# Kernel optimization log

Hardware: AMD Instinct MI355X
Metric: run time of the kernel (lower is better)

The kernel has to match this reference:

```python
import jax, jax.numpy as jnp
import numpy as np

D_MODEL = 1024
NUM_HEADS = 16
D_K = D_MODEL // NUM_HEADS
LOCAL_WINDOW = 16
LOCALITY_STRENGTH = 2.0


def _xavier(key, shape):
    fan_in, fan_out = shape[1], shape[0]
    a = jnp.sqrt(6.0 / (fan_in + fan_out))
    return jax.random.uniform(key, shape, jnp.float32, -a, a)


def setup_inputs() -> dict:
    key = jax.random.key(0)
    ks = jax.random.split(key, 9)
    B, S = 4, 2048
    query = jax.random.normal(ks[0], (B, S, D_MODEL), jnp.float32)
    key_t = jax.random.normal(ks[1], (B, S, D_MODEL), jnp.float32)
    value = jax.random.normal(ks[2], (B, S, D_MODEL), jnp.float32)
    wq = _xavier(ks[3], (D_MODEL, D_MODEL))
    wk = _xavier(ks[4], (D_MODEL, D_MODEL))
    wv = _xavier(ks[5], (D_MODEL, D_MODEL))
    wo = _xavier(ks[6], (D_MODEL, D_MODEL))
    bq = jnp.zeros((D_MODEL,), jnp.float32)
    bk = jnp.zeros((D_MODEL,), jnp.float32)
    bv = jnp.zeros((D_MODEL,), jnp.float32)
    bo = jnp.zeros((D_MODEL,), jnp.float32)
    # learned local relative-position bias, length 2*W+1; randomize so grads/math are nontrivial
    local_bias = 0.02 * jax.random.normal(ks[7], (2 * LOCAL_WINDOW + 1,), jnp.float32)
    return {"query": query, "key": key_t, "value": value,
            "wq": wq, "bq": bq, "wk": wk, "bk": bk, "wv": wv, "bv": bv,
            "wo": wo, "bo": bo, "local_bias": local_bias}


def _local_bias_matrix(local_bias, seq_len):
    # bias[i, j] = local_bias[j - i + W] if |j - i| <= W else 0  (banded)
    i = jnp.arange(seq_len)
    rel = i[None, :] - i[:, None]                 # [S, S]
    valid = jnp.abs(rel) <= LOCAL_WINDOW
    idx = jnp.clip(rel + LOCAL_WINDOW, 0, 2 * LOCAL_WINDOW)
    return jnp.where(valid, local_bias[idx], 0.0)  # [S, S]


def reference(query, key, value, wq, bq, wk, bk, wv, bv, wo, bo, local_bias):
    B, S, _ = query.shape
    H, Dk = NUM_HEADS, D_K
    q = (query @ wq.T + bq).reshape(B, S, H, Dk).transpose(0, 2, 1, 3)  # [B,H,S,Dk]
    k = (key @ wk.T + bk).reshape(B, S, H, Dk).transpose(0, 2, 1, 3)
    v = (value @ wv.T + bv).reshape(B, S, H, Dk).transpose(0, 2, 1, 3)
    scores = jnp.einsum('bhqd,bhkd->bhqk', q, k) / jnp.sqrt(jnp.float32(Dk))
    bias = _local_bias_matrix(local_bias, S)       # [S,S], broadcasts over [B,H]
    scores = scores + LOCALITY_STRENGTH * bias
    attn = jax.nn.softmax(scores, axis=-1)
    out = jnp.einsum('bhqk,bhkd->bhqd', attn, v)   # [B,H,S,Dk]
    out = out.transpose(0, 2, 1, 3).reshape(B, S, H * Dk)
    return out @ wo.T + bo
```

## Files before the change

### kernel.cpp

```cpp
#include <hip/hip_runtime.h>
#include <hip/hip_bf16.h>
#include <stdint.h>

typedef __bf16 bf16_t;
typedef bf16_t bf16x8 __attribute__((ext_vector_type(8)));
typedef bf16_t bf16x4 __attribute__((ext_vector_type(4)));
typedef float f32x4 __attribute__((ext_vector_type(4)));

#define LOG2E 1.44269504088896340736f

__device__ __forceinline__ void gld16(const void* g, void* l) {
  __builtin_amdgcn_global_load_lds(
      (__attribute__((address_space(1))) void*)(void*)(g),
      (__attribute__((address_space(3))) void*)(l), 16, 0, 0);
}

__device__ __forceinline__ int swz(int byteoff) {
  return byteoff ^ (((byteoff >> 7) & 7) << 4);
}

__global__ __launch_bounds__(256) void cvt7_kernel(
    const float* __restrict__ a0, const float* __restrict__ a1, const float* __restrict__ a2,
    const float* __restrict__ w0, const float* __restrict__ w1,
    const float* __restrict__ w2, const float* __restrict__ w3,
    bf16_t* __restrict__ e0, bf16_t* __restrict__ e1, bf16_t* __restrict__ e2,
    bf16_t* __restrict__ f0, bf16_t* __restrict__ f1,
    bf16_t* __restrict__ f2, bf16_t* __restrict__ f3) {
  const float* s;
  bf16_t* d;
  int i, stride;
  if (blockIdx.x < 3072) {
    const int t = blockIdx.x >> 10;
    s = (t == 0) ? a0 : ((t == 1) ? a1 : a2);
    d = (t == 0) ? e0 : ((t == 1) ? e1 : e2);
    i = (blockIdx.x & 1023) * 256 + threadIdx.x;
    stride = 1024 * 256;
  } else {
    const int b = blockIdx.x - 3072;
    const int t = b >> 7;
    s = (t == 0) ? w0 : ((t == 1) ? w1 : ((t == 2) ? w2 : w3));
    d = (t == 0) ? f0 : ((t == 1) ? f1 : ((t == 2) ? f2 : f3));
    i = (b & 127) * 256 + threadIdx.x;
    stride = 128 * 256;
  }
#pragma unroll
  for (int u = 0; u < 8; ++u, i += stride) {
    const float4 v = reinterpret_cast<const float4*>(s)[i];
    bf16x4 o;
    o[0] = (bf16_t)v.x; o[1] = (bf16_t)v.y; o[2] = (bf16_t)v.z; o[3] = (bf16_t)v.w;
    reinterpret_cast<bf16x4*>(d)[i] = o;
  }
}

#define GBM 128
#define GBN 128
#define GBK 64

__global__ __launch_bounds__(256) void gemm_qkv(
    const bf16_t* __restrict__ Xq, const bf16_t* __restrict__ Xk, const bf16_t* __restrict__ Xv,
    const bf16_t* __restrict__ Wq, const bf16_t* __restrict__ Wk, const bf16_t* __restrict__ Wv,
    const float* __restrict__ bq, const float* __restrict__ bk, const float* __restrict__ bv,
    bf16_t* __restrict__ Qo, bf16_t* __restrict__ Ko, bf16_t* __restrict__ Vo,
    int M, int N, int K) {
  const int z = blockIdx.z;
  const bf16_t* A = (z == 0) ? Xq : ((z == 1) ? Xk : Xv);
  const bf16_t* W = (z == 0) ? Wq : ((z == 1) ? Wk : Wv);
  const float* bias = (z == 0) ? bq : ((z == 1) ? bk : bv);
  bf16_t* Out = (z == 0) ? Qo : ((z == 1) ? Ko : Vo);

  __shared__ bf16_t As[GBM * GBK];
  __shared__ bf16_t Bs[GBN * GBK];
  const int tid = threadIdx.x;
  const int lane = tid & 63;
  const int w = tid >> 6;
  const int m0 = blockIdx.x * GBM;
  const int n0 = blockIdx.y * GBN;
  const int wm = (w >> 1) * 64;
  const int wn = (w & 1) * 64;

  f32x4 acc[4][4] = {};

  const int t16 = tid * 16;
  int srow[4], scb[4];
#pragma unroll
  for (int i = 0; i < 4; ++i) {
    const int so = swz(i * 4096 + t16);
    srow[i] = so >> 7;
    scb[i] = so & 127;
  }
  const char* Ab = (const char*)A;
  const char* Wb = (const char*)W;

  const int rr = lane & 15;
  const int kk8 = (lane >> 4) * 8;

  for (int k0 = 0; k0 < K; k0 += GBK) {
#pragma unroll
    for (int i = 0; i < 4; ++i) {
      gld16(Ab + ((size_t)(m0 + srow[i]) * K + k0) * 2 + scb[i], (char*)As + i * 4096 + t16);
      gld16(Wb + ((size_t)(n0 + srow[i]) * K + k0) * 2 + scb[i], (char*)Bs + i * 4096 + t16);
    }
    __syncthreads();
#pragma unroll
    for (int kk = 0; kk < 2; ++kk) {
      bf16x8 a[4], b[4];
#pragma unroll
      for (int i = 0; i < 4; ++i)
        a[i] = *reinterpret_cast<const bf16x8*>(
            (const char*)As + swz((wm + i * 16 + rr) * 128 + (kk * 32 + kk8) * 2));
#pragma unroll
      for (int i = 0; i < 4; ++i)
        b[i] = *reinterpret_cast<const bf16x8*>(
            (const char*)Bs + swz((wn + i * 16 + rr) * 128 + (kk * 32 + kk8) * 2));
#pragma unroll
      for (int i = 0; i < 4; ++i)
#pragma unroll
        for (int j = 0; j < 4; ++j)
          acc[i][j] = __builtin_amdgcn_mfma_f32_16x16x32_bf16(a[i], b[j], acc[i][j], 0, 0, 0);
    }
    __syncthreads();
  }

  const int rg = (lane >> 4) * 4;
#pragma unroll
  for (int i = 0; i < 4; ++i) {
#pragma unroll
    for (int j = 0; j < 4; ++j) {
      const int col = n0 + wn + j * 16 + rr;
      const float bi = bias[col];
      if (z == 2) {
        const int row0 = m0 + wm + i * 16 + rg;
        const int b_ = row0 >> 11, s_ = row0 & 2047;
        const int h_ = col >> 6, d_ = col & 63;
        const int k64 = s_ & 63;
        const int sl = (k64 & 32) | ((k64 & 12) << 1) | ((k64 & 16) >> 2);
        const int scol = (s_ & ~63) | sl;
        bf16x4 pack;
#pragma unroll
        for (int r = 0; r < 4; ++r) pack[r] = (bf16_t)(acc[i][j][r] + bi);
        *reinterpret_cast<bf16x4*>(&Out[((size_t)((b_ * 16 + h_) * 64 + d_)) * 2048 + scol]) = pack;
      } else {
        const float scale = (z == 0) ? (0.125f * LOG2E) : 1.0f;
#pragma unroll
        for (int r = 0; r < 4; ++r) {
          const int row = m0 + wm + i * 16 + rg + r;
          const int b_ = row >> 11, s_ = row & 2047;
          const int h_ = col >> 6, d_ = col & 63;
          Out[((size_t)((b_ * 16 + h_) * 2048 + s_)) * 64 + d_] = (bf16_t)((acc[i][j][r] + bi) * scale);
        }
      }
    }
  }
}

__global__ __launch_bounds__(256) void gemm_o(
    const bf16_t* __restrict__ A, const bf16_t* __restrict__ W,
    const float* __restrict__ bias, float* __restrict__ Out,
    int M, int N, int K) {
  __shared__ bf16_t As[GBM * GBK];
  __shared__ bf16_t Bs[GBN * GBK];
  const int tid = threadIdx.x;
  const int lane = tid & 63;
  const int w = tid >> 6;
  const int m0 = blockIdx.x * GBM;
  const int n0 = blockIdx.y * GBN;
  const int wm = (w >> 1) * 64;
  const int wn = (w & 1) * 64;

  f32x4 acc[4][4] = {};

  const int t16 = tid * 16;
  int srow[4], scb[4];
#pragma unroll
  for (int i = 0; i < 4; ++i) {
    const int so = swz(i * 4096 + t16);
    srow[i] = so >> 7;
    scb[i] = so & 127;
  }
  const char* Ab = (const char*)A;
  const char* Wb = (const char*)W;

  const int rr = lane & 15;
  const int kk8 = (lane >> 4) * 8;

  for (int k0 = 0; k0 < K; k0 += GBK) {
#pragma unroll
    for (int i = 0; i < 4; ++i) {
      gld16(Ab + ((size_t)(m0 + srow[i]) * K + k0) * 2 + scb[i], (char*)As + i * 4096 + t16);
      gld16(Wb + ((size_t)(n0 + srow[i]) * K + k0) * 2 + scb[i], (char*)Bs + i * 4096 + t16);
    }
    __syncthreads();
#pragma unroll
    for (int kk = 0; kk < 2; ++kk) {
      bf16x8 a[4], b[4];
#pragma unroll
      for (int i = 0; i < 4; ++i)
        a[i] = *reinterpret_cast<const bf16x8*>(
            (const char*)As + swz((wm + i * 16 + rr) * 128 + (kk * 32 + kk8) * 2));
#pragma unroll
      for (int i = 0; i < 4; ++i)
        b[i] = *reinterpret_cast<const bf16x8*>(
            (const char*)Bs + swz((wn + i * 16 + rr) * 128 + (kk * 32 + kk8) * 2));
#pragma unroll
      for (int i = 0; i < 4; ++i)
#pragma unroll
        for (int j = 0; j < 4; ++j)
          acc[i][j] = __builtin_amdgcn_mfma_f32_16x16x32_bf16(a[i], b[j], acc[i][j], 0, 0, 0);
    }
    __syncthreads();
  }

  const int rg = (lane >> 4) * 4;
#pragma unroll
  for (int i = 0; i < 4; ++i)
#pragma unroll
    for (int j = 0; j < 4; ++j) {
      const int col = n0 + wn + j * 16 + rr;
      const float bi = bias[col];
#pragma unroll
      for (int r = 0; r < 4; ++r) {
        const int row = m0 + wm + i * 16 + rg + r;
        Out[(size_t)row * N + col] = acc[i][j][r] + bi;
      }
    }
}

#define QT 256
#define KT 64

__global__ __launch_bounds__(256, 2) void attn_kernel(
    const bf16_t* __restrict__ Qg, const bf16_t* __restrict__ Kg,
    const bf16_t* __restrict__ Vtg, const float* __restrict__ lb,
    bf16_t* __restrict__ Og) {
  const int S = 2048;
  __shared__ bf16_t Qs[QT * 64];
  __shared__ bf16_t Ks[KT * 64];
  __shared__ bf16_t Vts[64 * KT];
  __shared__ float lbs[33];

  const int tid = threadIdx.x, lane = tid & 63, w = tid >> 6;
  const int bh = blockIdx.x;
  const int qt0 = blockIdx.y * QT;
  const int b_ = bh >> 4, h_ = bh & 15;

  const char* Qb = (const char*)(Qg + (size_t)bh * S * 64);
  const char* Kb = (const char*)(Kg + (size_t)bh * S * 64);
  const char* Vtb = (const char*)(Vtg + (size_t)bh * 64 * S);

#pragma unroll
  for (int i = 0; i < 8; ++i) {
    const int off = i * 4096 + tid * 16;
    gld16(Qb + (size_t)qt0 * 128 + swz(off), (char*)Qs + off);
  }
  if (tid < 33) lbs[tid] = lb[tid];

  const int L0 = tid * 16;
  const int W0 = swz(L0), W1 = swz(L0 + 4096);
  const int vd0 = L0 >> 7, vcb = L0 & 127;
  int4 kr0, kr1, vr0, vr1;

#define LOADKV(t)                                                              \
  {                                                                            \
    const char* kp = Kb + (size_t)(t) * 8192;                                  \
    kr0 = *reinterpret_cast<const int4*>(kp + L0);                             \
    kr1 = *reinterpret_cast<const int4*>(kp + L0 + 4096);                      \
    const char* vp = Vtb + (size_t)(t) * 128;                                  \
    vr0 = *reinterpret_cast<const int4*>(vp + (size_t)vd0 * 4096 + vcb);       \
    vr1 = *reinterpret_cast<const int4*>(vp + (size_t)(vd0 + 32) * 4096 + vcb);\
  }
#define WRITEKV()                                                              \
  {                                                                            \
    *reinterpret_cast<int4*>((char*)Ks + W0) = kr0;                            \
    *reinterpret_cast<int4*>((char*)Ks + W1) = kr1;                            \
    *reinterpret_cast<int4*>((char*)Vts + W0) = vr0;                           \
    *reinterpret_cast<int4*>((char*)Vts + W1) = vr1;                           \
  }

  LOADKV(0)
  __syncthreads();

  const int rr = lane & 15;
  const int kk8 = (lane >> 4) * 8;
  const int rg = (lane >> 4) * 4;

  bf16x8 qf[4][2];
#pragma unroll
  for (int qg = 0; qg < 4; ++qg)
#pragma unroll
    for (int kk = 0; kk < 2; ++kk) {
      const int off = (w * 64 + qg * 16 + rr) * 128 + (kk * 32 + kk8) * 2;
      qf[qg][kk] = *reinterpret_cast<const bf16x8*>((const char*)Qs + swz(off));
    }

  f32x4 oacc[4][4] = {};
  float lrowp[4] = {0.f, 0.f, 0.f, 0.f};

  for (int kt = 0; kt < S / KT; ++kt) {
    WRITEKV()
    __syncthreads();
    LOADKV((kt + 1) & 31)

    bf16x8 kf[4][2];
#pragma unroll
    for (int ni = 0; ni < 4; ++ni)
#pragma unroll
      for (int kk = 0; kk < 2; ++kk) {
        const int off = (ni * 16 + rr) * 128 + (kk * 32 + kk8) * 2;
        kf[ni][kk] = *reinterpret_cast<const bf16x8*>((const char*)Ks + swz(off));
      }
    bf16x8 vf[2][4];
#pragma unroll
    for (int kk = 0; kk < 2; ++kk)
#pragma unroll
      for (int nd = 0; nd < 4; ++nd) {
        const int off = (nd * 16 + rr) * 128 + (kk * 32 + kk8) * 2;
        vf[kk][nd] = *reinterpret_cast<const bf16x8*>((const char*)Vts + swz(off));
      }

    const int kbase = kt * KT;
#pragma unroll
    for (int qg = 0; qg < 4; ++qg) {
      f32x4 sc[4];
      __builtin_amdgcn_s_setprio(1);
#pragma unroll
      for (int ni = 0; ni < 4; ++ni) {
        f32x4 z = {0.f, 0.f, 0.f, 0.f};
#pragma unroll
        for (int kk = 0; kk < 2; ++kk)
          z = __builtin_amdgcn_mfma_f32_16x16x32_bf16(kf[ni][kk], qf[qg][kk], z, 0, 0, 0);
        sc[ni] = z;
      }
      __builtin_amdgcn_s_setprio(0);

      const int qlo = qt0 + w * 64 + qg * 16;
      if (kbase + KT + 16 > qlo && kbase < qlo + 16 + 16) {
        const int q = qlo + rr;
#pragma unroll
        for (int ni = 0; ni < 4; ++ni)
#pragma unroll
          for (int r = 0; r < 4; ++r) {
            const int rel = (kbase + ni * 16 + rg + r) - q;
            if (rel >= -16 && rel <= 16)
              sc[ni][r] += (2.0f * LOG2E) * lbs[rel + 16];
          }
      }

      bf16x8 paf[2];
      float ps0 = 0.f, ps1 = 0.f;
#pragma unroll
      for (int ni = 0; ni < 4; ++ni) {
        const float p0 = exp2f(sc[ni][0]);
        const float p1 = exp2f(sc[ni][1]);
        const float p2 = exp2f(sc[ni][2]);
        const float p3 = exp2f(sc[ni][3]);
        ps0 += p0 + p2;
        ps1 += p1 + p3;
        paf[ni >> 1][(ni & 1) * 4 + 0] = (bf16_t)p0;
        paf[ni >> 1][(ni & 1) * 4 + 1] = (bf16_t)p1;
        paf[ni >> 1][(ni & 1) * 4 + 2] = (bf16_t)p2;
        paf[ni >> 1][(ni & 1) * 4 + 3] = (bf16_t)p3;
      }
      lrowp[qg] += ps0 + ps1;

      __builtin_amdgcn_s_setprio(1);
#pragma unroll
      for (int kk = 0; kk < 2; ++kk)
#pragma unroll
        for (int nd = 0; nd < 4; ++nd)
          oacc[qg][nd] = __builtin_amdgcn_mfma_f32_16x16x32_bf16(paf[kk], vf[kk][nd], oacc[qg][nd], 0, 0, 0);
      __builtin_amdgcn_s_setprio(0);
    }
    __syncthreads();
  }

#pragma unroll
  for (int qg = 0; qg < 4; ++qg) {
    float t = lrowp[qg];
    t += __shfl_xor(t, 16, 64);
    t += __shfl_xor(t, 32, 64);
    float lf[4];
#pragma unroll
    for (int r = 0; r < 4; ++r)
      lf[r] = __shfl(t, (lane & 48) | (rg + r), 64);
#pragma unroll
    for (int nd = 0; nd < 4; ++nd)
#pragma unroll
      for (int r = 0; r < 4; ++r) {
        const int srow = qt0 + w * 64 + qg * 16 + rg + r;
        const int d = nd * 16 + rr;
        const float v = oacc[qg][nd][r] / lf[r];
        Og[((size_t)(b_ * 2048 + srow)) * 1024 + h_ * 64 + d] = (bf16_t)v;
      }
  }
}

extern "C" void kernel_launch(void* const* d_in, const int* in_sizes, int n_in,
                              void* d_out, int out_size, void* d_ws, size_t ws_size,
                              hipStream_t stream) {
  const float* q32 = (const float*)d_in[0];
  const float* k32 = (const float*)d_in[1];
  const float* v32 = (const float*)d_in[2];
  const float* wq = (const float*)d_in[3];
  const float* bq = (const float*)d_in[4];
  const float* wk = (const float*)d_in[5];
  const float* bk = (const float*)d_in[6];
  const float* wv = (const float*)d_in[7];
  const float* bv = (const float*)d_in[8];
  const float* wo = (const float*)d_in[9];
  const float* bo = (const float*)d_in[10];
  const float* lb = (const float*)d_in[11];

  const int M = 8192, N = 1024, K = 1024;
  const size_t REG = (size_t)M * N * 2;

  char* ws = (char*)d_ws;
  bf16_t* Xq = (bf16_t*)(ws + 0 * REG);
  bf16_t* Xk = (bf16_t*)(ws + 1 * REG);
  bf16_t* Xv = (bf16_t*)(ws + 2 * REG);
  bf16_t* Qb = (bf16_t*)(ws + 3 * REG);
  bf16_t* Wqb = (bf16_t*)(ws + 4 * REG);
  bf16_t* Wkb = Wqb + (size_t)N * K;
  bf16_t* Wvb = Wkb + (size_t)N * K;
  bf16_t* Wob = Wvb + (size_t)N * K;
  bf16_t* Kb = Xq;
  bf16_t* Vt = Xk;
  bf16_t* attn = Xv;

  cvt7_kernel<<<dim3(3584), dim3(256), 0, stream>>>(
      q32, k32, v32, wq, wk, wv, wo, Xq, Xk, Xv, Wqb, Wkb, Wvb, Wob);

  gemm_qkv<<<dim3(M / GBM, N / GBN, 3), 256, 0, stream>>>(
      Xq, Xk, Xv, Wqb, Wkb, Wvb, bq, bk, bv, Qb, Kb, Vt, M, N, K);

  attn_kernel<<<dim3(64, 2048 / QT), 256, 0, stream>>>(Qb, Kb, Vt, lb, attn);

  gemm_o<<<dim3(M / GBM, N / GBN), 256, 0, stream>>>(attn, Wob, bo, (float*)d_out, M, N, K);
}
```

Before: 240.9 us.

## Double-buffer LDS tiles in projection GEMMs to overlap loads with MFMA

Both projection GEMMs now share a core routine that uses two LDS buffers per operand. The next K-tile is prefetched with global_load_lds while MFMAs run on the current tile, and one barrier per iteration replaces two. It also raises wave priority around the MFMA block. On the last iteration the loop issues a wrapped-around redundant prefetch, and LDS use doubles to 64KB per block, which may lower occupancy.

```diff
diff --git a/kernel.cpp b/kernel.cpp
--- a/kernel.cpp
+++ b/kernel.cpp
@@ -56,6 +56,66 @@
 #define GBN 128
 #define GBK 64
 
+__device__ __forceinline__ void gemm_core(
+    const bf16_t* __restrict__ A, const bf16_t* __restrict__ W,
+    bf16_t* As, bf16_t* Bs, int m0, int n0, int K,
+    int wm, int wn, int rr, int kk8, f32x4 acc[4][4]) {
+  const int tid = threadIdx.x;
+  const int t16 = tid * 16;
+  int srow[4], scb[4];
+#pragma unroll
+  for (int i = 0; i < 4; ++i) {
+    const int so = swz(i * 4096 + t16);
+    srow[i] = so >> 7;
+    scb[i] = so & 127;
+  }
+  const char* Ab = (const char*)A;
+  const char* Wb = (const char*)W;
+  const int nk = K / GBK;
+
+#define GSTAGE(bufsel, kk0)                                                    \
+  {                                                                            \
+    char* Al = (char*)As + (bufsel) * 16384 + t16;                             \
+    char* Bl = (char*)Bs + (bufsel) * 16384 + t16;                             \
+    _Pragma("unroll")                                                          \
+    for (int i = 0; i < 4; ++i) {                                              \
+      gld16(Ab + ((size_t)(m0 + srow[i]) * K + (kk0)) * 2 + scb[i], Al + i * 4096); \
+      gld16(Wb + ((size_t)(n0 + srow[i]) * K + (kk0)) * 2 + scb[i], Bl + i * 4096); \
+    }                                                                          \
+  }
+
+  GSTAGE(0, 0)
+  for (int t = 0; t < nk; ++t) {
+    const int b = t & 1;
+    asm volatile("s_waitcnt vmcnt(0)" ::: "memory");
+    __builtin_amdgcn_s_barrier();
+    __builtin_amdgcn_sched_barrier(0);
+    GSTAGE(b ^ 1, ((t + 1) & (nk - 1)) * GBK)
+    const char* Abl = (const char*)As + b * 16384;
+    const char* Bbl = (const char*)Bs + b * 16384;
+#pragma unroll
+    for (int kk = 0; kk < 2; ++kk) {
+      bf16x8 a[4], bb[4];
+#pragma unroll
+      for (int i = 0; i < 4; ++i)
+        a[i] = *reinterpret_cast<const bf16x8*>(
+            Abl + swz((wm + i * 16 + rr) * 128 + (kk * 32 + kk8) * 2));
+#pragma unroll
+      for (int i = 0; i < 4; ++i)
+        bb[i] = *reinterpret_cast<const bf16x8*>(
+            Bbl + swz((wn + i * 16 + rr) * 128 + (kk * 32 + kk8) * 2));
+      __builtin_amdgcn_s_setprio(1);
+#pragma unroll
+      for (int i = 0; i < 4; ++i)
+#pragma unroll
+        for (int j = 0; j < 4; ++j)
+          acc[i][j] = __builtin_amdgcn_mfma_f32_16x16x32_bf16(a[i], bb[j], acc[i][j], 0, 0, 0);
+      __builtin_amdgcn_s_setprio(0);
+    }
+  }
+#undef GSTAGE
+}
+
 __global__ __launch_bounds__(256) void gemm_qkv(
     const bf16_t* __restrict__ Xq, const bf16_t* __restrict__ Xk, const bf16_t* __restrict__ Xv,
     const bf16_t* __restrict__ Wq, const bf16_t* __restrict__ Wk, const bf16_t* __restrict__ Wv,
@@ -68,8 +128,8 @@
   const float* bias = (z == 0) ? bq : ((z == 1) ? bk : bv);
   bf16_t* Out = (z == 0) ? Qo : ((z == 1) ? Ko : Vo);
 
-  __shared__ bf16_t As[GBM * GBK];
-  __shared__ bf16_t Bs[GBN * GBK];
+  __shared__ bf16_t As[2 * GBM * GBK];
+  __shared__ bf16_t Bs[2 * GBN * GBK];
   const int tid = threadIdx.x;
   const int lane = tid & 63;
   const int w = tid >> 6;
@@ -77,49 +137,11 @@
   const int n0 = blockIdx.y * GBN;
   const int wm = (w >> 1) * 64;
   const int wn = (w & 1) * 64;
-
-  f32x4 acc[4][4] = {};
-
-  const int t16 = tid * 16;
-  int srow[4], scb[4];
-#pragma unroll
-  for (int i = 0; i < 4; ++i) {
-    const int so = swz(i * 4096 + t16);
-    srow[i] = so >> 7;
-    scb[i] = so & 127;
-  }
-  const char* Ab = (const char*)A;
-  const char* Wb = (const char*)W;
-
   const int rr = lane & 15;
   const int kk8 = (lane >> 4) * 8;
 
-  for (int k0 = 0; k0 < K; k0 += GBK) {
-#pragma unroll
-    for (int i = 0; i < 4; ++i) {
-      gld16(Ab + ((size_t)(m0 + srow[i]) * K + k0) * 2 + scb[i], (char*)As + i * 4096 + t16);
-      gld16(Wb + ((size_t)(n0 + srow[i]) * K + k0) * 2 + scb[i], (char*)Bs + i * 4096 + t16);
-    }
-    __syncthreads();
-#pragma unroll
-    for (int kk = 0; kk < 2; ++kk) {
-      bf16x8 a[4], b[4];
-#pragma unroll
-      for (int i = 0; i < 4; ++i)
-        a[i] = *reinterpret_cast<const bf16x8*>(
-            (const char*)As + swz((wm + i * 16 + rr) * 128 + (kk * 32 + kk8) * 2));
-#pragma unroll
-      for (int i = 0; i < 4; ++i)
-        b[i] = *reinterpret_cast<const bf16x8*>(
-            (const char*)Bs + swz((wn + i * 16 + rr) * 128 + (kk * 32 + kk8) * 2));
-#pragma unroll
-      for (int i = 0; i < 4; ++i)
-#pragma unroll
-        for (int j = 0; j < 4; ++j)
-          acc[i][j] = __builtin_amdgcn_mfma_f32_16x16x32_bf16(a[i], b[j], acc[i][j], 0, 0, 0);
-    }
-    __syncthreads();
-  }
+  f32x4 acc[4][4] = {};
+  gemm_core(A, W, As, Bs, m0, n0, K, wm, wn, rr, kk8, acc);
 
   const int rg = (lane >> 4) * 4;
 #pragma unroll
@@ -157,8 +179,8 @@
     const bf16_t* __restrict__ A, const bf16_t* __restrict__ W,
     const float* __restrict__ bias, float* __restrict__ Out,
     int M, int N, int K) {
-  __shared__ bf16_t As[GBM * GBK];
-  __shared__ bf16_t Bs[GBN * GBK];
+  __shared__ bf16_t As[2 * GBM * GBK];
+  __shared__ bf16_t Bs[2 * GBN * GBK];
   const int tid = threadIdx.x;
   const int lane = tid & 63;
   const int w = tid >> 6;
@@ -166,49 +188,11 @@
   const int n0 = blockIdx.y * GBN;
   const int wm = (w >> 1) * 64;
   const int wn = (w & 1) * 64;
-
-  f32x4 acc[4][4] = {};
-
-  const int t16 = tid * 16;
-  int srow[4], scb[4];
-#pragma unroll
-  for (int i = 0; i < 4; ++i) {
-    const int so = swz(i * 4096 + t16);
-    srow[i] = so >> 7;
-    scb[i] = so & 127;
-  }
-  const char* Ab = (const char*)A;
-  const char* Wb = (const char*)W;
-
   const int rr = lane & 15;
   const int kk8 = (lane >> 4) * 8;
 
-  for (int k0 = 0; k0 < K; k0 += GBK) {
-#pragma unroll
-    for (int i = 0; i < 4; ++i) {
-      gld16(Ab + ((size_t)(m0 + srow[i]) * K + k0) * 2 + scb[i], (char*)As + i * 4096 + t16);
-      gld16(Wb + ((size_t)(n0 + srow[i]) * K + k0) * 2 + scb[i], (char*)Bs + i * 4096 + t16);
-    }
-    __syncthreads();
-#pragma unroll
-    for (int kk = 0; kk < 2; ++kk) {
-      bf16x8 a[4], b[4];
-#pragma unroll
-      for (int i = 0; i < 4; ++i)
-        a[i] = *reinterpret_cast<const bf16x8*>(
-            (const char*)As + swz((wm + i * 16 + rr) * 128 + (kk * 32 + kk8) * 2));
-#pragma unroll
-      for (int i = 0; i < 4; ++i)
-        b[i] = *reinterpret_cast<const bf16x8*>(
-            (const char*)Bs + swz((wn + i * 16 + rr) * 128 + (kk * 32 + kk8) * 2));
-#pragma unroll
-      for (int i = 0; i < 4; ++i)
-#pragma unroll
-        for (int j = 0; j < 4; ++j)
-          acc[i][j] = __builtin_amdgcn_mfma_f32_16x16x32_bf16(a[i], b[j], acc[i][j], 0, 0, 0);
-    }
-    __syncthreads();
-  }
+  f32x4 acc[4][4] = {};
+  gemm_core(A, W, As, Bs, m0, n0, K, wm, wn, rr, kk8, acc);
 
   const int rg = (lane >> 4) * 4;
 #pragma unroll
```

New measurement: 229.8 us. 1.05x faster.
